# Kernel optimization log

Hardware: AMD Instinct MI355X
Metric: run time of the kernel (lower is better)

## Reference

```python
import jax, jax.numpy as jnp
import numpy as np

N_NODES = 20000
N_EDGES = 480000
HIDDEN = 128
EDGE_FEAT = 128
BN_EPS = 1e-5


def setup_inputs() -> dict:
    key = jax.random.key(0)
    ks = jax.random.split(key, 6)
    z_dim = 2 * HIDDEN + EDGE_FEAT
    h = jax.random.normal(ks[0], (N_NODES, HIDDEN), dtype=jnp.float32)
    e = jax.random.normal(ks[1], (N_EDGES, EDGE_FEAT), dtype=jnp.float32)
    src = jax.random.randint(ks[2], (N_EDGES,), 0, N_NODES, dtype=jnp.int32)
    dst = jax.random.randint(ks[3], (N_EDGES,), 0, N_NODES, dtype=jnp.int32)
    W = jax.random.normal(ks[4], (z_dim, 2 * HIDDEN), dtype=jnp.float32) / np.sqrt(z_dim)
    b = jax.random.normal(ks[5], (2 * HIDDEN,), dtype=jnp.float32) * 0.01
    gamma = jnp.ones((2 * HIDDEN,), dtype=jnp.float32)
    beta = jnp.zeros((2 * HIDDEN,), dtype=jnp.float32)
    return {"h": h, "e": e, "src": src, "dst": dst, "W": W, "b": b,
            "gamma": gamma, "beta": beta}


def reference(h, e, src, dst, W, b, gamma, beta):
    # Gather endpoint features per edge: z = [h_src, h_dst, e]  -> [E, z_dim]
    z = jnp.concatenate([h[src], h[dst], e], axis=1)
    # Linear
    z = z @ W + b  # [E, 2*HIDDEN]
    # BatchNorm1d over the edge batch (training-mode stats, biased variance)
    mean = jnp.mean(z, axis=0)
    var = jnp.mean(jnp.square(z - mean), axis=0)
    z = (z - mean) * jax.lax.rsqrt(var + BN_EPS) * gamma + beta
    # Gated softplus message
    nbr_filter, nbr_core = jnp.split(z, 2, axis=1)
    msg = jax.nn.sigmoid(nbr_filter) * jax.nn.softplus(nbr_core)  # [E, HIDDEN]
    # Segment-sum reduce into destination nodes
    agg = jax.ops.segment_sum(msg, dst, num_segments=N_NODES)  # [N, HIDDEN]
    # Residual + softplus (dropout=0.0)
    return jax.nn.softplus(h + agg)
```

## Files before the change

kernel.cpp:

```cpp
#include <hip/hip_runtime.h>
#include <hip/hip_bf16.h>
#include <math.h>

#define N_NODES 20000
#define N_EDGES 480000
#define HIDDEN  128
#define ZDIM    384
#define NOUT    256
#define BN_EPS  1e-5f

#define LDA     392
#define LDZ     264

using bf16x8 = __attribute__((ext_vector_type(8))) short;
using f32x4  = __attribute__((ext_vector_type(4))) float;
using f32x16 = __attribute__((ext_vector_type(16))) float;
using s16x4  = __attribute__((ext_vector_type(4))) short;

struct f32x8 { float4 a, b; };

__device__ __forceinline__ unsigned short f2b(float f) {
    union { float f; unsigned u; } v; v.f = f;
    unsigned r = v.u + 0x7fffu + ((v.u >> 16) & 1u);
    return (unsigned short)(r >> 16);
}
__device__ __forceinline__ float bflo(unsigned u) {
    union { unsigned x; float f; } v; v.x = u << 16; return v.f;
}
__device__ __forceinline__ float bfhi(unsigned u) {
    union { unsigned x; float f; } v; v.x = u & 0xffff0000u; return v.f;
}
__device__ __forceinline__ float b2f(unsigned short s) {
    union { unsigned u; float f; } v; v.u = ((unsigned)s) << 16; return v.f;
}
__device__ __forceinline__ float sigmoid_(float x) {
    return 1.f / (1.f + __expf(-x));
}
__device__ __forceinline__ float softplus_(float x) {
    return fmaxf(x, 0.f) + __logf(1.f + __expf(-fabsf(x)));
}
__device__ __forceinline__ f32x8 ld8(const float* p) {
    f32x8 r; r.a = *(const float4*)p; r.b = *(const float4*)(p + 4); return r;
}
__device__ __forceinline__ bf16x8 cvt8(f32x8 v) {
    bf16x8 pk;
    pk[0] = (short)f2b(v.a.x); pk[1] = (short)f2b(v.a.y);
    pk[2] = (short)f2b(v.a.z); pk[3] = (short)f2b(v.a.w);
    pk[4] = (short)f2b(v.b.x); pk[5] = (short)f2b(v.b.y);
    pk[6] = (short)f2b(v.b.z); pk[7] = (short)f2b(v.b.w);
    return pk;
}

__global__ void convW(const float* __restrict__ W, short* __restrict__ wt) {
    int n = blockIdx.x;
    for (int k = threadIdx.x; k < ZDIM; k += 256)
        wt[n * ZDIM + k] = (short)f2b(W[(size_t)k * NOUT + n]);
}

__global__ void bn_finalize(const float* __restrict__ stats,
                            const float* __restrict__ gamma,
                            const float* __restrict__ beta,
                            float* __restrict__ scaleC,
                            float* __restrict__ shiftC) {
    int c = threadIdx.x;
    float s = 0.f, q = 0.f;
    for (int p = 0; p < 64; ++p) {
        s += stats[p * 512 + c];
        q += stats[p * 512 + 256 + c];
    }
    const float invE = 1.f / (float)N_EDGES;
    float m   = s * invE;
    float var = q * invE - m * m;
    float inv = rsqrtf(var + BN_EPS);
    float sc  = gamma[c] * inv;
    scaleC[c] = sc;
    shiftC[c] = beta[c] - m * sc;
}

__global__ void hist_dst(const int* __restrict__ dst, int* __restrict__ counts) {
    int i = blockIdx.x * 256 + threadIdx.x;
    if (i < N_EDGES) atomicAdd(&counts[dst[i]], 1);
}

__global__ void scan_nodes(const int* __restrict__ counts, int* __restrict__ offs,
                           int* __restrict__ cursor) {
    __shared__ int part[1024];
    int t = threadIdx.x;
    int base = t * 20;
    int local[20]; int s = 0;
    #pragma unroll
    for (int k = 0; k < 20; ++k) {
        int idx = base + k;
        int v = (idx < N_NODES) ? counts[idx] : 0;
        local[k] = s; s += v;
    }
    part[t] = s; __syncthreads();
    for (int d = 1; d < 1024; d <<= 1) {
        int v = (t >= d) ? part[t - d] : 0;
        __syncthreads();
        part[t] += v;
        __syncthreads();
    }
    int pre = (t > 0) ? part[t - 1] : 0;
    #pragma unroll
    for (int k = 0; k < 20; ++k) {
        int idx = base + k;
        if (idx < N_NODES) { int o = pre + local[k]; offs[idx] = o; cursor[idx] = o; }
    }
}

__global__ void build_ipos(const int* __restrict__ dst, int* __restrict__ cursor,
                           int* __restrict__ ipos) {
    int i = blockIdx.x * 256 + threadIdx.x;
    if (i < N_EDGES) ipos[i] = atomicAdd(&cursor[dst[i]], 1);
}

__global__ __launch_bounds__(256)
void node_proj(const float* __restrict__ h, const short* __restrict__ wt,
               unsigned short* __restrict__ P1, unsigned short* __restrict__ P2) {
    const int tid  = threadIdx.x;
    const int lane = tid & 63;
    const int l31  = lane & 31;
    const int hi   = lane >> 5;
    const int w    = tid >> 6;
    const int rowBase = blockIdx.x * 64;
    const int colBase = blockIdx.y * 256 + w * 64;

    const float* pA[2];
    #pragma unroll
    for (int mi = 0; mi < 2; ++mi) {
        int row = rowBase + mi * 32 + l31;
        if (row > N_NODES - 1) row = N_NODES - 1;
        pA[mi] = h + (size_t)row * HIDDEN + hi * 8;
    }
    const short* pB[2];
    #pragma unroll
    for (int n = 0; n < 2; ++n) {
        int c = colBase + n * 32 + l31;
        pB[n] = wt + (size_t)(c & 255) * ZDIM + (c >> 8) * 128 + hi * 8;
    }

    f32x16 acc[2][2] = {};
    #pragma unroll
    for (int kk = 0; kk < 8; ++kk) {
        bf16x8 a[2], b[2];
        #pragma unroll
        for (int mi = 0; mi < 2; ++mi) a[mi] = cvt8(ld8(pA[mi] + kk * 16));
        #pragma unroll
        for (int n = 0; n < 2; ++n) b[n] = *(const bf16x8*)(pB[n] + kk * 16);
        #pragma unroll
        for (int mi = 0; mi < 2; ++mi)
            #pragma unroll
            for (int n = 0; n < 2; ++n)
                acc[mi][n] = __builtin_amdgcn_mfma_f32_32x32x16_bf16(
                                 a[mi], b[n], acc[mi][n], 0, 0, 0);
    }

    unsigned short* Pt = (blockIdx.y == 0) ? P1 : P2;
    const int pcol = (w * 64) + l31 * 2;
    #pragma unroll
    for (int mi = 0; mi < 2; ++mi)
        #pragma unroll
        for (int r = 0; r < 16; ++r) {
            int row = rowBase + mi * 32 + 4 * hi + (r & 3) + 8 * (r >> 2);
            if (row < N_NODES) {
                unsigned pk = (unsigned)f2b(acc[mi][0][r]) |
                              ((unsigned)f2b(acc[mi][1][r]) << 16);
                *(unsigned*)&Pt[(size_t)row * 256 + pcol] = pk;
            }
        }
}

__global__ __launch_bounds__(256, 3)
void edge_gemm3(const float* __restrict__ e, const int* __restrict__ src,
                const int* __restrict__ dst, const short* __restrict__ wt,
                const int* __restrict__ ipos,
                const unsigned short* __restrict__ P1,
                const unsigned short* __restrict__ P2,
                float* __restrict__ stats, short* __restrict__ zout) {
    const int tid  = threadIdx.x;
    const int lane = tid & 63;
    const int l31  = lane & 31;
    const int hi   = lane >> 5;
    const int w    = tid >> 6;
    const int rowBase = blockIdx.x * 64;
    const int colBase = w * 64;
    const int pcol = colBase + l31 * 2;

    const float* pE[2];
    #pragma unroll
    for (int mi = 0; mi < 2; ++mi)
        pE[mi] = e + (size_t)(rowBase + mi * 32 + l31) * HIDDEN + hi * 8;
    const short* pB[2];
    #pragma unroll
    for (int n = 0; n < 2; ++n)
        pB[n] = wt + (size_t)(colBase + n * 32 + l31) * ZDIM + 256 + hi * 8;

    f32x8 t[2][4];
    bf16x8 A0[2][4], A1[2][4];
    #pragma unroll
    for (int mi = 0; mi < 2; ++mi)
        #pragma unroll
        for (int j = 0; j < 4; ++j) t[mi][j] = ld8(pE[mi] + j * 16);
    #pragma unroll
    for (int mi = 0; mi < 2; ++mi)
        #pragma unroll
        for (int j = 0; j < 4; ++j) A0[mi][j] = cvt8(t[mi][j]);
    #pragma unroll
    for (int mi = 0; mi < 2; ++mi)
        #pragma unroll
        for (int j = 0; j < 4; ++j) t[mi][j] = ld8(pE[mi] + 64 + j * 16);

    f32x16 acc[2][2] = {};
    bf16x8 bC[2], bN[2];
    #pragma unroll
    for (int n = 0; n < 2; ++n) bC[n] = *(const bf16x8*)(pB[n]);

    #pragma unroll
    for (int kk = 0; kk < 4; ++kk) {
        #pragma unroll
        for (int n = 0; n < 2; ++n) bN[n] = *(const bf16x8*)(pB[n] + (kk + 1) * 16);
        #pragma unroll
        for (int mi = 0; mi < 2; ++mi)
            #pragma unroll
            for (int n = 0; n < 2; ++n)
                acc[mi][n] = __builtin_amdgcn_mfma_f32_32x32x16_bf16(
                                 A0[mi][kk], bC[n], acc[mi][n], 0, 0, 0);
        #pragma unroll
        for (int n = 0; n < 2; ++n) bC[n] = bN[n];
    }
    #pragma unroll
    for (int mi = 0; mi < 2; ++mi)
        #pragma unroll
        for (int j = 0; j < 4; ++j) A1[mi][j] = cvt8(t[mi][j]);
    #pragma unroll
    for (int kk = 4; kk < 8; ++kk) {
        if (kk < 7) {
            #pragma unroll
            for (int n = 0; n < 2; ++n) bN[n] = *(const bf16x8*)(pB[n] + (kk + 1) * 16);
        }
        #pragma unroll
        for (int mi = 0; mi < 2; ++mi)
            #pragma unroll
            for (int n = 0; n < 2; ++n)
                acc[mi][n] = __builtin_amdgcn_mfma_f32_32x32x16_bf16(
                                 A1[mi][kk - 4], bC[n], acc[mi][n], 0, 0, 0);
        if (kk < 7) {
            #pragma unroll
            for (int n = 0; n < 2; ++n) bC[n] = bN[n];
        }
    }

    float s2[2] = {0.f, 0.f}, q2[2] = {0.f, 0.f};
    #pragma unroll
    for (int mi = 0; mi < 2; ++mi) {
        #pragma unroll
        for (int r = 0; r < 16; ++r) {
            int rowL = mi * 32 + 4 * hi + (r & 3) + 8 * (r >> 2);
            int g    = rowBase + rowL;
            int sI   = src[g];
            int dI   = dst[g];
            int slot = ipos[g];
            unsigned ps = *(const unsigned*)&P1[(size_t)sI * 256 + pcol];
            unsigned pd = *(const unsigned*)&P2[(size_t)dI * 256 + pcol];
            float z0 = acc[mi][0][r] + bflo(ps) + bflo(pd);
            float z1 = acc[mi][1][r] + bfhi(ps) + bfhi(pd);
            s2[0] += z0; q2[0] += z0 * z0;
            s2[1] += z1; q2[1] += z1 * z1;
            short* zp = (short*)&zout[(size_t)slot * NOUT + colBase];
            zp[l31]      = (short)f2b(z0);
            zp[32 + l31] = (short)f2b(z1);
        }
    }
    float* base = stats + (size_t)(blockIdx.x & 63) * 512;
    #pragma unroll
    for (int n = 0; n < 2; ++n) {
        float s = s2[n], q = q2[n];
        s += __shfl_xor(s, 32, 64);
        q += __shfl_xor(q, 32, 64);
        if (lane < 32) {
            int col = colBase + n * 32 + l31;
            atomicAdd(base + col, s);
            atomicAdd(base + 256 + col, q);
        }
    }
}

template<int MODE>
__global__ __launch_bounds__(256)
void edge_gemm_fb(const float* __restrict__ h, const float* __restrict__ e,
                  const int* __restrict__ src, const int* __restrict__ dst,
                  const short* __restrict__ wt,
                  float* __restrict__ stats,
                  const float* __restrict__ scaleC, const float* __restrict__ shiftC,
                  float* __restrict__ agg) {
    const int tid  = threadIdx.x;
    const int bm   = blockIdx.x;
    const int rowBase = bm * 64;
    const int lane = tid & 63;
    const int brow = lane & 15;
    const int kgo  = (lane >> 4) * 8;
    const int wcol = (tid >> 6) * 64;

    __shared__ __align__(16) short lds[64 * LDA];

    #pragma unroll
    for (int j = 0; j < 12; ++j) {
        int u = tid + j * 256;
        int r = u / 48;
        int f0 = (u - r * 48) * 8;
        int row = rowBase + r;
        const float* p;
        if (f0 < 128)      p = h + (size_t)src[row] * HIDDEN + f0;
        else if (f0 < 256) p = h + (size_t)dst[row] * HIDDEN + (f0 - 128);
        else               p = e + (size_t)row * HIDDEN + (f0 - 256);
        *(bf16x8*)&lds[r * LDA + f0] = cvt8(ld8(p));
    }
    __syncthreads();

    const short* wB[4];
    #pragma unroll
    for (int n = 0; n < 4; ++n)
        wB[n] = wt + (size_t)(wcol + n * 16 + brow) * ZDIM + kgo;

    f32x4 acc[4][4] = {};
    #pragma unroll
    for (int kk = 0; kk < 12; ++kk) {
        bf16x8 aC[4], bC[4];
        #pragma unroll
        for (int m = 0; m < 4; ++m)
            aC[m] = *(const bf16x8*)&lds[(m * 16 + brow) * LDA + kk * 32 + kgo];
        #pragma unroll
        for (int n = 0; n < 4; ++n) bC[n] = *(const bf16x8*)(wB[n] + kk * 32);
        #pragma unroll
        for (int m = 0; m < 4; ++m)
            #pragma unroll
            for (int n = 0; n < 4; ++n)
                acc[m][n] = __builtin_amdgcn_mfma_f32_16x16x32_bf16(
                                aC[m], bC[n], acc[m][n], 0, 0, 0);
    }

    if (MODE == 1) {
        float* base = stats + (size_t)(bm & 63) * 512;
        #pragma unroll
        for (int n = 0; n < 4; ++n) {
            float s = 0.f, q = 0.f;
            #pragma unroll
            for (int m = 0; m < 4; ++m)
                #pragma unroll
                for (int r = 0; r < 4; ++r) {
                    float v = acc[m][n][r]; s += v; q += v * v;
                }
            s += __shfl_xor(s, 16, 64); s += __shfl_xor(s, 32, 64);
            q += __shfl_xor(q, 16, 64); q += __shfl_xor(q, 32, 64);
            if (lane < 16) {
                int col = wcol + n * 16 + lane;
                atomicAdd(base + col, s);
                atomicAdd(base + 256 + col, q);
            }
        }
    } else {
        float sc[4], sh[4];
        #pragma unroll
        for (int n = 0; n < 4; ++n) {
            int col = wcol + n * 16 + brow;
            sc[n] = scaleC[col]; sh[n] = shiftC[col];
        }
        __syncthreads();
        #pragma unroll
        for (int m = 0; m < 4; ++m) {
            int rowb = m * 16 + (lane >> 4) * 4;
            #pragma unroll
            for (int n = 0; n < 4; ++n) {
                int col = wcol + n * 16 + brow;
                #pragma unroll
                for (int r = 0; r < 4; ++r)
                    lds[(rowb + r) * LDZ + col] = (short)f2b(acc[m][n][r] * sc[n] + sh[n]);
            }
        }
        __syncthreads();
        const int c0 = (tid & 31) * 4;
        const int r0 = tid >> 5;
        #pragma unroll
        for (int rp = 0; rp < 8; ++rp) {
            int row = rp * 8 + r0;
            int d   = dst[rowBase + row];
            float* ap = agg + (size_t)d * HIDDEN + c0;
            s16x4 f4 = *(const s16x4*)&lds[row * LDZ + c0];
            s16x4 c4 = *(const s16x4*)&lds[row * LDZ + 128 + c0];
            #pragma unroll
            for (int j = 0; j < 4; ++j)
                atomicAdd(ap + j, sigmoid_(b2f((unsigned short)f4[j])) *
                                  softplus_(b2f((unsigned short)c4[j])));
        }
    }
}

__global__ __launch_bounds__(256)
void node_gather(const short* __restrict__ z,
                 const int* __restrict__ offs, const int* __restrict__ counts,
                 const float* __restrict__ scaleC, const float* __restrict__ shiftC,
                 const float* __restrict__ h, float* __restrict__ out) {
    int node = blockIdx.x * 4 + (threadIdx.x >> 6);
    int lane = threadIdx.x & 63;
    int l32  = lane & 31;
    int c0   = l32 * 4;

    float scF[4], shF[4], scS[4], shS[4];
    #pragma unroll
    for (int k = 0; k < 4; ++k) {
        scF[k] = scaleC[c0 + k];       shF[k] = shiftC[c0 + k];
        scS[k] = scaleC[128 + c0 + k]; shS[k] = shiftC[128 + c0 + k];
    }

    int s   = offs[node];
    int deg = counts[node];
    float a0 = 0.f, a1 = 0.f, a2 = 0.f, a3 = 0.f;

    for (int j = (lane >> 5); j < deg; j += 4) {
        int jB = j + 2;
        bool hasB = (jB < deg);
        const short* zA = z + (size_t)(s + j) * NOUT + c0;
        const short* zB = z + (size_t)(s + (hasB ? jB : j)) * NOUT + c0;
        uint2 fA = *(const uint2*)zA;
        uint2 cA = *(const uint2*)(zA + 128);
        uint2 fB = *(const uint2*)zB;
        uint2 cB = *(const uint2*)(zB + 128);

        float f0 = bflo(fA.x) * scF[0] + shF[0];
        float f1 = bfhi(fA.x) * scF[1] + shF[1];
        float f2 = bflo(fA.y) * scF[2] + shF[2];
        float f3 = bfhi(fA.y) * scF[3] + shF[3];
        float g0 = bflo(cA.x) * scS[0] + shS[0];
        float g1 = bfhi(cA.x) * scS[1] + shS[1];
        float g2 = bflo(cA.y) * scS[2] + shS[2];
        float g3 = bfhi(cA.y) * scS[3] + shS[3];
        a0 += sigmoid_(f0) * softplus_(g0);
        a1 += sigmoid_(f1) * softplus_(g1);
        a2 += sigmoid_(f2) * softplus_(g2);
        a3 += sigmoid_(f3) * softplus_(g3);

        if (hasB) {
            f0 = bflo(fB.x) * scF[0] + shF[0];
            f1 = bfhi(fB.x) * scF[1] + shF[1];
            f2 = bflo(fB.y) * scF[2] + shF[2];
            f3 = bfhi(fB.y) * scF[3] + shF[3];
            g0 = bflo(cB.x) * scS[0] + shS[0];
            g1 = bfhi(cB.x) * scS[1] + shS[1];
            g2 = bflo(cB.y) * scS[2] + shS[2];
            g3 = bfhi(cB.y) * scS[3] + shS[3];
            a0 += sigmoid_(f0) * softplus_(g0);
            a1 += sigmoid_(f1) * softplus_(g1);
            a2 += sigmoid_(f2) * softplus_(g2);
            a3 += sigmoid_(f3) * softplus_(g3);
        }
    }
    a0 += __shfl_xor(a0, 32, 64);
    a1 += __shfl_xor(a1, 32, 64);
    a2 += __shfl_xor(a2, 32, 64);
    a3 += __shfl_xor(a3, 32, 64);

    if (lane < 32) {
        size_t o = (size_t)node * HIDDEN + c0;
        float4 hv = *(const float4*)&h[o];
        float4 r;
        r.x = softplus_(hv.x + a0);
        r.y = softplus_(hv.y + a1);
        r.z = softplus_(hv.z + a2);
        r.w = softplus_(hv.w + a3);
        *(float4*)&out[o] = r;
    }
}

__global__ void node_finalize(const float* __restrict__ h, float* __restrict__ out) {
    int i = blockIdx.x * 256 + threadIdx.x;
    float4 hv = ((const float4*)h)[i];
    float4 av = ((float4*)out)[i];
    float4 r;
    r.x = softplus_(hv.x + av.x);
    r.y = softplus_(hv.y + av.y);
    r.z = softplus_(hv.z + av.z);
    r.w = softplus_(hv.w + av.w);
    ((float4*)out)[i] = r;
}

extern "C" void kernel_launch(void* const* d_in, const int* in_sizes, int n_in,
                              void* d_out, int out_size, void* d_ws, size_t ws_size,
                              hipStream_t stream) {
    const float* h     = (const float*)d_in[0];
    const float* e     = (const float*)d_in[1];
    const int*   srcp  = (const int*)d_in[2];
    const int*   dstp  = (const int*)d_in[3];
    const float* W     = (const float*)d_in[4];
    const float* gamma = (const float*)d_in[6];
    const float* beta  = (const float*)d_in[7];
    float* out = (float*)d_out;

    char*  ws     = (char*)d_ws;
    float* stats  = (float*)ws;
    float* scaleC = (float*)(ws + 131072);
    float* shiftC = (float*)(ws + 132096);
    short* wt     = (short*)(ws + 133120);
    int*   counts = (int*)(ws + 329728);
    int*   offs   = (int*)(ws + 409856);
    int*   cursor = (int*)(ws + 489984);
    int*   ipos   = (int*)(ws + 570112);
    unsigned short* P1 = (unsigned short*)(ws + 2490112);
    unsigned short* P2 = (unsigned short*)(ws + 12730112);
    short* zbuf   = (short*)(ws + 22970112);
    const size_t need = 22970112ull + (size_t)N_EDGES * NOUT * 2;

    hipMemsetAsync(stats, 0, 131072, stream);
    convW<<<NOUT, 256, 0, stream>>>(W, wt);

    if (ws_size >= need) {
        hipMemsetAsync(counts, 0, N_NODES * sizeof(int), stream);
        hist_dst<<<(N_EDGES + 255) / 256, 256, 0, stream>>>(dstp, counts);
        scan_nodes<<<1, 1024, 0, stream>>>(counts, offs, cursor);
        build_ipos<<<(N_EDGES + 255) / 256, 256, 0, stream>>>(dstp, cursor, ipos);

        node_proj<<<dim3((N_NODES + 63) / 64, 2), 256, 0, stream>>>(h, wt, P1, P2);
        edge_gemm3<<<N_EDGES / 64, 256, 0, stream>>>(e, srcp, dstp, wt, ipos,
                P1, P2, stats, zbuf);
        bn_finalize<<<1, 256, 0, stream>>>(stats, gamma, beta, scaleC, shiftC);
        node_gather<<<N_NODES / 4, 256, 0, stream>>>(zbuf, offs, counts,
                scaleC, shiftC, h, out);
    } else {
        hipMemsetAsync(out, 0, (size_t)N_NODES * HIDDEN * sizeof(float), stream);
        edge_gemm_fb<1><<<N_EDGES / 64, 256, 0, stream>>>(h, e, srcp, dstp, wt,
                stats, nullptr, nullptr, nullptr);
        bn_finalize<<<1, 256, 0, stream>>>(stats, gamma, beta, scaleC, shiftC);
        edge_gemm_fb<2><<<N_EDGES / 64, 256, 0, stream>>>(h, e, srcp, dstp, wt,
                stats, scaleC, shiftC, out);
        node_finalize<<<N_NODES * HIDDEN / (4 * 256), 256, 0, stream>>>(h, out);
    }
}
```

Baseline: 485.2 us.

## Pack z stores as interleaved column pairs and batch gathers in edge GEMM

The edge GEMM now writes each z row as packed 32-bit pairs of columns (c, c+32) in an interleaved layout, instead of two scattered 16-bit stores. node_gather is changed to read that permuted layout and remap its scale/shift and output columns to match. The edge kernel also preloads all B fragments up front and issues every src/dst/P1/P2 gather before the epilogue math, so the loads can overlap. To make room for the extra registers this needs, the occupancy hint drops from 3 to 2 blocks per SM, which lowers latency hiding.

New measurement: 472.7 us. 2.6% less time.

```diff
diff --git a/kernel.cpp b/kernel.cpp
--- a/kernel.cpp
+++ b/kernel.cpp
@@ -171,7 +171,7 @@
         }
 }
 
-__global__ __launch_bounds__(256, 3)
+__global__ __launch_bounds__(256, 2)
 void edge_gemm3(const float* __restrict__ e, const int* __restrict__ src,
                 const int* __restrict__ dst, const short* __restrict__ wt,
                 const int* __restrict__ ipos,
@@ -197,14 +197,21 @@
         pB[n] = wt + (size_t)(colBase + n * 32 + l31) * ZDIM + 256 + hi * 8;
 
     f32x8 t[2][4];
+    #pragma unroll
+    for (int mi = 0; mi < 2; ++mi)
+        #pragma unroll
+        for (int j = 0; j < 4; ++j) t[mi][j] = ld8(pE[mi] + j * 16);
+    bf16x8 B[2][8];
+    #pragma unroll
+    for (int n = 0; n < 2; ++n)
+        #pragma unroll
+        for (int kk = 0; kk < 8; ++kk)
+            B[n][kk] = *(const bf16x8*)(pB[n] + kk * 16);
+
     bf16x8 A0[2][4], A1[2][4];
     #pragma unroll
     for (int mi = 0; mi < 2; ++mi)
         #pragma unroll
-        for (int j = 0; j < 4; ++j) t[mi][j] = ld8(pE[mi] + j * 16);
-    #pragma unroll
-    for (int mi = 0; mi < 2; ++mi)
-        #pragma unroll
         for (int j = 0; j < 4; ++j) A0[mi][j] = cvt8(t[mi][j]);
     #pragma unroll
     for (int mi = 0; mi < 2; ++mi)
@@ -212,66 +219,54 @@
         for (int j = 0; j < 4; ++j) t[mi][j] = ld8(pE[mi] + 64 + j * 16);
 
     f32x16 acc[2][2] = {};
-    bf16x8 bC[2], bN[2];
-    #pragma unroll
-    for (int n = 0; n < 2; ++n) bC[n] = *(const bf16x8*)(pB[n]);
-
-    #pragma unroll
-    for (int kk = 0; kk < 4; ++kk) {
-        #pragma unroll
-        for (int n = 0; n < 2; ++n) bN[n] = *(const bf16x8*)(pB[n] + (kk + 1) * 16);
+    #pragma unroll
+    for (int kk = 0; kk < 4; ++kk)
         #pragma unroll
         for (int mi = 0; mi < 2; ++mi)
             #pragma unroll
             for (int n = 0; n < 2; ++n)
                 acc[mi][n] = __builtin_amdgcn_mfma_f32_32x32x16_bf16(
-                                 A0[mi][kk], bC[n], acc[mi][n], 0, 0, 0);
-        #pragma unroll
-        for (int n = 0; n < 2; ++n) bC[n] = bN[n];
-    }
+                                 A0[mi][kk], B[n][kk], acc[mi][n], 0, 0, 0);
     #pragma unroll
     for (int mi = 0; mi < 2; ++mi)
         #pragma unroll
         for (int j = 0; j < 4; ++j) A1[mi][j] = cvt8(t[mi][j]);
     #pragma unroll
-    for (int kk = 4; kk < 8; ++kk) {
-        if (kk < 7) {
-            #pragma unroll
-            for (int n = 0; n < 2; ++n) bN[n] = *(const bf16x8*)(pB[n] + (kk + 1) * 16);
-        }
+    for (int kk = 4; kk < 8; ++kk)
         #pragma unroll
         for (int mi = 0; mi < 2; ++mi)
             #pragma unroll
             for (int n = 0; n < 2; ++n)
                 acc[mi][n] = __builtin_amdgcn_mfma_f32_32x32x16_bf16(
-                                 A1[mi][kk - 4], bC[n], acc[mi][n], 0, 0, 0);
-        if (kk < 7) {
-            #pragma unroll
-            for (int n = 0; n < 2; ++n) bC[n] = bN[n];
-        }
-    }
-
-    float s2[2] = {0.f, 0.f}, q2[2] = {0.f, 0.f};
-    #pragma unroll
-    for (int mi = 0; mi < 2; ++mi) {
+                                 A1[mi][kk - 4], B[n][kk], acc[mi][n], 0, 0, 0);
+
+    unsigned ps[2][16], pd[2][16];
+    int slot[2][16];
+    #pragma unroll
+    for (int mi = 0; mi < 2; ++mi)
         #pragma unroll
         for (int r = 0; r < 16; ++r) {
             int rowL = mi * 32 + 4 * hi + (r & 3) + 8 * (r >> 2);
             int g    = rowBase + rowL;
             int sI   = src[g];
             int dI   = dst[g];
-            int slot = ipos[g];
-            unsigned ps = *(const unsigned*)&P1[(size_t)sI * 256 + pcol];
-            unsigned pd = *(const unsigned*)&P2[(size_t)dI * 256 + pcol];
-            float z0 = acc[mi][0][r] + bflo(ps) + bflo(pd);
-            float z1 = acc[mi][1][r] + bfhi(ps) + bfhi(pd);
+            slot[mi][r] = ipos[g];
+            ps[mi][r] = *(const unsigned*)&P1[(size_t)sI * 256 + pcol];
+            pd[mi][r] = *(const unsigned*)&P2[(size_t)dI * 256 + pcol];
+        }
+
+    float s2[2] = {0.f, 0.f}, q2[2] = {0.f, 0.f};
+    #pragma unroll
+    for (int mi = 0; mi < 2; ++mi)
+        #pragma unroll
+        for (int r = 0; r < 16; ++r) {
+            float z0 = acc[mi][0][r] + bflo(ps[mi][r]) + bflo(pd[mi][r]);
+            float z1 = acc[mi][1][r] + bfhi(ps[mi][r]) + bfhi(pd[mi][r]);
             s2[0] += z0; q2[0] += z0 * z0;
             s2[1] += z1; q2[1] += z1 * z1;
-            short* zp = (short*)&zout[(size_t)slot * NOUT + colBase];
-            zp[l31]      = (short)f2b(z0);
-            zp[32 + l31] = (short)f2b(z1);
-        }
-    }
+            unsigned pk = (unsigned)f2b(z0) | ((unsigned)f2b(z1) << 16);
+            *(unsigned*)&zout[(size_t)slot[mi][r] * NOUT + pcol] = pk;
+        }
     float* base = stats + (size_t)(blockIdx.x & 63) * 512;
     #pragma unroll
     for (int n = 0; n < 2; ++n) {
@@ -404,28 +399,31 @@
     int node = blockIdx.x * 4 + (threadIdx.x >> 6);
     int lane = threadIdx.x & 63;
     int l32  = lane & 31;
-    int c0   = l32 * 4;
+    const int wq = l32 >> 4;
+    const int c0 = 64 * wq + 2 * (l32 & 15);
 
     float scF[4], shF[4], scS[4], shS[4];
+    const int cmap[4] = {c0, c0 + 32, c0 + 1, c0 + 33};
     #pragma unroll
     for (int k = 0; k < 4; ++k) {
-        scF[k] = scaleC[c0 + k];       shF[k] = shiftC[c0 + k];
-        scS[k] = scaleC[128 + c0 + k]; shS[k] = shiftC[128 + c0 + k];
+        scF[k] = scaleC[cmap[k]];       shF[k] = shiftC[cmap[k]];
+        scS[k] = scaleC[128 + cmap[k]]; shS[k] = shiftC[128 + cmap[k]];
     }
 
     int s   = offs[node];
     int deg = counts[node];
     float a0 = 0.f, a1 = 0.f, a2 = 0.f, a3 = 0.f;
+    const int po = 4 * l32;
 
     for (int j = (lane >> 5); j < deg; j += 4) {
         int jB = j + 2;
         bool hasB = (jB < deg);
-        const short* zA = z + (size_t)(s + j) * NOUT + c0;
-        const short* zB = z + (size_t)(s + (hasB ? jB : j)) * NOUT + c0;
-        uint2 fA = *(const uint2*)zA;
-        uint2 cA = *(const uint2*)(zA + 128);
-        uint2 fB = *(const uint2*)zB;
-        uint2 cB = *(const uint2*)(zB + 128);
+        const short* zA = z + (size_t)(s + j) * NOUT;
+        const short* zB = z + (size_t)(s + (hasB ? jB : j)) * NOUT;
+        uint2 fA = *(const uint2*)(zA + po);
+        uint2 cA = *(const uint2*)(zA + 128 + po);
+        uint2 fB = *(const uint2*)(zB + po);
+        uint2 cB = *(const uint2*)(zB + 128 + po);
 
         float f0 = bflo(fA.x) * scF[0] + shF[0];
         float f1 = bfhi(fA.x) * scF[1] + shF[1];
@@ -461,14 +459,16 @@
     a3 += __shfl_xor(a3, 32, 64);
 
     if (lane < 32) {
-        size_t o = (size_t)node * HIDDEN + c0;
-        float4 hv = *(const float4*)&h[o];
-        float4 r;
-        r.x = softplus_(hv.x + a0);
-        r.y = softplus_(hv.y + a1);
-        r.z = softplus_(hv.z + a2);
-        r.w = softplus_(hv.w + a3);
-        *(float4*)&out[o] = r;
+        size_t o = (size_t)node * HIDDEN;
+        float2 hA = *(const float2*)&h[o + c0];
+        float2 hB = *(const float2*)&h[o + c0 + 32];
+        float2 rA, rB;
+        rA.x = softplus_(hA.x + a0);
+        rA.y = softplus_(hA.y + a2);
+        rB.x = softplus_(hB.x + a1);
+        rB.y = softplus_(hB.y + a3);
+        *(float2*)&out[o + c0]      = rA;
+        *(float2*)&out[o + c0 + 32] = rB;
     }
 }
 
```
